# Kernel tuning notes

Hardware: AMD Instinct MI355X
Metric: run time of the kernel (lower is better)

The kernel has to match this reference:

```python
import jax, jax.numpy as jnp
import numpy as np

N_NODES = 50000
N_EDGES = 800000
NFEAT, NHID, NCLASS = 512, 128, 40


def _glorot(key, fan_in, fan_out):
    # mimics the usual GCN uniform init: U(-1/sqrt(fan_out), 1/sqrt(fan_out))
    stdv = 1.0 / np.sqrt(fan_out)
    return jax.random.uniform(key, (fan_in, fan_out), jnp.float32, -stdv, stdv)


def setup_inputs() -> dict:
    key = jax.random.key(0)
    ks = jax.random.split(key, 8)
    x = jax.random.normal(ks[0], (N_NODES, NFEAT), jnp.float32)
    edge_src = jax.random.randint(ks[1], (N_EDGES,), 0, N_NODES)
    edge_dst = jax.random.randint(ks[2], (N_EDGES,), 0, N_NODES)
    edge_weight = jax.random.uniform(ks[3], (N_EDGES,), jnp.float32)
    W1 = _glorot(ks[4], NFEAT, NHID)
    b1 = jnp.zeros((NHID,), jnp.float32)
    W2 = _glorot(ks[5], NHID, NCLASS)
    b2 = jnp.zeros((NCLASS,), jnp.float32)
    return {"x": x, "edge_src": edge_src, "edge_dst": edge_dst,
            "edge_weight": edge_weight, "W1": W1, "b1": b1, "W2": W2, "b2": b2}


def _gcn_layer(x, W, b, edge_src, edge_dst, edge_weight):
    # support = x @ W ; out = spmm(adj, support) + b
    support = x @ W                                   # [N, F_out]
    msgs = support[edge_src] * edge_weight[:, None]   # [E, F_out]
    agg = jax.ops.segment_sum(msgs, edge_dst, num_segments=N_NODES)
    return agg + b


def reference(x, edge_src, edge_dst, edge_weight, W1, b1, W2, b2):
    h = _gcn_layer(x, W1, b1, edge_src, edge_dst, edge_weight)
    h = jax.nn.relu(h)
    # F.dropout(training=False) -> identity in eval mode
    out = _gcn_layer(h, W2, b2, edge_src, edge_dst, edge_weight)
    return out
```

## Files before the change

### kernel.cpp

```cpp
#include <hip/hip_runtime.h>


#define F0 512
#define F1 128
#define F2 40
#define F2P 48

typedef short bf16x8 __attribute__((ext_vector_type(8)));
typedef float f32x4 __attribute__((ext_vector_type(4)));

static __device__ __forceinline__ unsigned short f2b(float f){
    union { float f; unsigned int u; } x; x.f = f;
    unsigned int u = x.u;
    unsigned int r = (u + 0x7fffu + ((u >> 16) & 1u)) >> 16;
    return (unsigned short)r;
}
static __device__ __forceinline__ unsigned short f2b_fast(float f){
    return (unsigned short)((__float_as_uint(f) + 0x8000u) >> 16);
}
static __device__ __forceinline__ unsigned int pack2(float a, float b){
    unsigned int ua = __float_as_uint(a) + 0x8000u;
    unsigned int ub = __float_as_uint(b) + 0x8000u;
    return __builtin_amdgcn_perm(ub, ua, 0x07060302u);
}
static __device__ __forceinline__ bf16x8 pack8(float4 v0, float4 v1){
    union { bf16x8 v; unsigned int d[4]; } r;
    r.d[0] = pack2(v0.x, v0.y);
    r.d[1] = pack2(v0.z, v0.w);
    r.d[2] = pack2(v1.x, v1.y);
    r.d[3] = pack2(v1.z, v1.w);
    return r.v;
}
static __device__ __forceinline__ float b2f(unsigned short h){
    union { unsigned int u; float f; } x; x.u = ((unsigned int)h) << 16; return x.f;
}
static __device__ __forceinline__ unsigned short f2h(float f){
    union { _Float16 h; unsigned short u; } x; x.h = (_Float16)f; return x.u;
}
static __device__ __forceinline__ float h2f(unsigned short u){
    union { unsigned short u; _Float16 h; } x; x.u = u; return (float)x.h;
}

__global__ void prep_w(const float* __restrict__ W1, const float* __restrict__ W2,
                       unsigned short* __restrict__ W1t, unsigned short* __restrict__ W2t,
                       int* __restrict__ cnt8, int n8){
    int idx = blockIdx.x*256 + threadIdx.x;
    if (idx < n8) cnt8[idx] = 0;
    if (idx < F0*F1){
        int k = idx >> 7, n = idx & 127;
        W1t[(size_t)n*F0 + k] = f2b(W1[idx]);
    } else if (idx < F0*F1 + F2P*F1){
        int j = idx - F0*F1;
        int n = j >> 7, k = j & 127;
        float v = (n < F2) ? W2[(size_t)k*F2 + n] : 0.f;
        W2t[j] = f2b(v);
    }
}

__global__ void hist_kernel(const int* __restrict__ dst, int* __restrict__ cnt8,
                            unsigned short* __restrict__ slot, int E){
    int e = blockIdx.x*256 + threadIdx.x;
    if (e < E){
        int d = dst[e];
        int s = e & 7;
        slot[e] = (unsigned short)atomicAdd(&cnt8[d*8 + s], 1);
    }
}

__global__ void scan1_kernel(const int* __restrict__ cnt8, int* __restrict__ offs,
                             unsigned short* __restrict__ lsp, int* __restrict__ bsum, int n){
    __shared__ int sd[256];
    int tid = threadIdx.x;
    int base = blockIdx.x*1024 + tid*4;
    int t[4];
    #pragma unroll
    for (int j=0;j<4;j++){
        int node = base+j;
        int tot = 0;
        if (node < n){
            int4 c0 = *(const int4*)&cnt8[(size_t)node*8];
            int4 c1 = *(const int4*)&cnt8[(size_t)node*8+4];
            unsigned short lp0=0, lp1, lp2, lp3, lp4, lp5, lp6, lp7;
            int run = c0.x; lp1=(unsigned short)run;
            run += c0.y; lp2=(unsigned short)run;
            run += c0.z; lp3=(unsigned short)run;
            run += c0.w; lp4=(unsigned short)run;
            run += c1.x; lp5=(unsigned short)run;
            run += c1.y; lp6=(unsigned short)run;
            run += c1.z; lp7=(unsigned short)run;
            run += c1.w; tot = run;
            ushort4 a, b;
            a.x=lp0; a.y=lp1; a.z=lp2; a.w=lp3;
            b.x=lp4; b.y=lp5; b.z=lp6; b.w=lp7;
            *(ushort4*)&lsp[(size_t)node*8]   = a;
            *(ushort4*)&lsp[(size_t)node*8+4] = b;
        }
        t[j] = tot;
    }
    int v1=t[0], v2=t[0]+t[1], v3=v2+t[2];
    int s = v3+t[3];
    sd[tid]=s; __syncthreads();
    for (int off=1; off<256; off<<=1){
        int tt = (tid>=off)? sd[tid-off] : 0;
        __syncthreads();
        sd[tid] += tt;
        __syncthreads();
    }
    int excl = sd[tid] - s;
    if (base+0<n) offs[base+0]=excl;
    if (base+1<n) offs[base+1]=excl+v1;
    if (base+2<n) offs[base+2]=excl+v2;
    if (base+3<n) offs[base+3]=excl+v3;
    if (tid==255) bsum[blockIdx.x]=sd[255];
}

__global__ void scan3_kernel(int* __restrict__ offs, int* __restrict__ sbase,
                             const unsigned short* __restrict__ lsp,
                             const int* __restrict__ bsum, int n, int E, int nb){
    __shared__ int sexcl;
    int tid = threadIdx.x;
    if (tid < 64){
        int v = (tid < nb) ? bsum[tid] : 0;
        int orig = v;
        #pragma unroll
        for (int off=1; off<64; off<<=1){
            int t = __shfl_up(v, off);
            if (tid >= off) v += t;
        }
        int g = blockIdx.x >> 2;
        if (tid == g) sexcl = v - orig;
    }
    __syncthreads();
    int i = blockIdx.x*256 + tid;
    if (i<n){
        int o = offs[i] + sexcl;
        offs[i] = o;
        ushort4 a = *(const ushort4*)&lsp[(size_t)i*8];
        ushort4 b = *(const ushort4*)&lsp[(size_t)i*8+4];
        int4 s0, s1;
        s0.x=o+a.x; s0.y=o+a.y; s0.z=o+a.z; s0.w=o+a.w;
        s1.x=o+b.x; s1.y=o+b.y; s1.z=o+b.z; s1.w=o+b.w;
        *(int4*)&sbase[(size_t)i*8]   = s0;
        *(int4*)&sbase[(size_t)i*8+4] = s1;
    }
    if (i==0) offs[n]=E;
}

__global__ void scatter_kernel(const int* __restrict__ src, const int* __restrict__ dst,
                               const float* __restrict__ w,
                               const int* __restrict__ sbase,
                               const unsigned short* __restrict__ slot,
                               unsigned int* __restrict__ edges, int E){
    int e = blockIdx.x*256+threadIdx.x;
    if (e<E){
        int d = dst[e];
        int pos = sbase[d*8 + (e & 7)] + (int)slot[e];
        edges[pos] = ((unsigned int)src[e] << 16) | (unsigned int)f2h(w[e]);
    }
}

__global__ __launch_bounds__(256) void gemm1_mfma(const float* __restrict__ X,
                                                  const unsigned short* __restrict__ W1t,
                                                  unsigned short* __restrict__ S1, int M){
    __shared__ unsigned short sB[128*136];
    int tid = threadIdx.x;
    int wave = tid >> 6, lane = tid & 63;
    int quad = lane >> 4, l16 = lane & 15;
    int row0 = blockIdx.x * 64;
    int myrow = row0 + wave*16 + l16;
    int arow = min(myrow, M-1);
    const float* xrow = X + (size_t)arow * F0;

    f32x4 acc[8];
    #pragma unroll
    for (int c=0;c<8;c++) acc[c] = (f32x4){0.f,0.f,0.f,0.f};

    float4 aq[4][2];
    #pragma unroll
    for (int s=0;s<4;s++){
        aq[s][0] = *(const float4*)(xrow + s*32 + quad*8);
        aq[s][1] = *(const float4*)(xrow + s*32 + quad*8 + 4);
    }

    for (int p = 0; p < 4; p++){
        __syncthreads();
        #pragma unroll
        for (int i=0;i<8;i++){
            int idx = tid + i*256;
            int nn = idx >> 4, c8 = idx & 15;
            *(float4*)&sB[nn*136 + c8*8] =
                *(const float4*)&W1t[(size_t)nn*F0 + p*128 + c8*8];
        }
        __syncthreads();
        float4 nq[4][2];
        if (p < 3){
            const float* nx = xrow + (p+1)*128;
            #pragma unroll
            for (int s=0;s<4;s++){
                nq[s][0] = *(const float4*)(nx + s*32 + quad*8);
                nq[s][1] = *(const float4*)(nx + s*32 + quad*8 + 4);
            }
        }
        #pragma unroll
        for (int s=0;s<4;s++){
            bf16x8 af = pack8(aq[s][0], aq[s][1]);
            #pragma unroll
            for (int c=0;c<8;c++){
                bf16x8 b = *(bf16x8*)&sB[(c*16 + l16)*136 + s*32 + quad*8];
                acc[c] = __builtin_amdgcn_mfma_f32_16x16x32_bf16(af, b, acc[c], 0, 0, 0);
            }
        }
        if (p < 3){
            #pragma unroll
            for (int s=0;s<4;s++){ aq[s][0]=nq[s][0]; aq[s][1]=nq[s][1]; }
        }
    }
    #pragma unroll
    for (int c=0;c<8;c++){
        #pragma unroll
        for (int r=0;r<4;r++){
            int grow = row0 + wave*16 + quad*4 + r;
            if (grow < M) S1[(size_t)grow*F1 + c*16 + l16] = f2b_fast(acc[c][r]);
        }
    }
}

__global__ void agg1_kernel(const unsigned short* __restrict__ S1, const int* __restrict__ offs,
                            const unsigned int* __restrict__ edges,
                            const float* __restrict__ b1, unsigned short* __restrict__ H, int n){
    int node = blockIdx.x*4 + (threadIdx.x >> 6);
    int lane = threadIdx.x & 63;
    if (node >= n) return;
    int half = lane >> 5, fl = lane & 31;
    int e0 = offs[node], e1 = offs[node+1];
    double a0=0.0, a1=0.0, a2=0.0, a3=0.0;
    int e = e0;
    for (; e+8 <= e1; e += 8){
        unsigned int rA = edges[e   + half];
        unsigned int rB = edges[e+2 + half];
        unsigned int rC = edges[e+4 + half];
        unsigned int rD = edges[e+6 + half];
        ushort4 vA = *(const ushort4*)&S1[((size_t)(rA>>16))*F1 + fl*4];
        ushort4 vB = *(const ushort4*)&S1[((size_t)(rB>>16))*F1 + fl*4];
        ushort4 vC = *(const ushort4*)&S1[((size_t)(rC>>16))*F1 + fl*4];
        ushort4 vD = *(const ushort4*)&S1[((size_t)(rD>>16))*F1 + fl*4];
        double wA = h2f((unsigned short)rA), wB = h2f((unsigned short)rB);
        double wC = h2f((unsigned short)rC), wD = h2f((unsigned short)rD);
        a0 += wA*b2f(vA.x) + wB*b2f(vB.x) + wC*b2f(vC.x) + wD*b2f(vD.x);
        a1 += wA*b2f(vA.y) + wB*b2f(vB.y) + wC*b2f(vC.y) + wD*b2f(vD.y);
        a2 += wA*b2f(vA.z) + wB*b2f(vB.z) + wC*b2f(vC.z) + wD*b2f(vD.z);
        a3 += wA*b2f(vA.w) + wB*b2f(vB.w) + wC*b2f(vC.w) + wD*b2f(vD.w);
    }
    for (; e < e1; e += 2){
        int ee = e + half;
        if (ee < e1){
            unsigned int r = edges[ee];
            ushort4 v = *(const ushort4*)&S1[((size_t)(r>>16))*F1 + fl*4];
            double w = h2f((unsigned short)r);
            a0 += w*b2f(v.x); a1 += w*b2f(v.y); a2 += w*b2f(v.z); a3 += w*b2f(v.w);
        }
    }
    a0 += __shfl_down(a0, 32);
    a1 += __shfl_down(a1, 32);
    a2 += __shfl_down(a2, 32);
    a3 += __shfl_down(a3, 32);
    if (lane < 32){
        float4 bb = *(const float4*)&b1[fl*4];
        float o0 = (float)(a0 + (double)bb.x);
        float o1 = (float)(a1 + (double)bb.y);
        float o2 = (float)(a2 + (double)bb.z);
        float o3 = (float)(a3 + (double)bb.w);
        o0 = o0>0.f?o0:0.f; o1 = o1>0.f?o1:0.f;
        o2 = o2>0.f?o2:0.f; o3 = o3>0.f?o3:0.f;
        union { ushort4 v; unsigned int d[2]; } o;
        o.d[0] = pack2(o0, o1);
        o.d[1] = pack2(o2, o3);
        *(ushort4*)&H[(size_t)node*F1 + fl*4] = o.v;
    }
}

__global__ __launch_bounds__(256) void gemm2_mfma(const unsigned short* __restrict__ H,
                                                  const unsigned short* __restrict__ W2t,
                                                  unsigned short* __restrict__ S2, int M){
    __shared__ unsigned short sB[48][136];
    int tid = threadIdx.x;
    int wave = tid >> 6, lane = tid & 63;
    int quad = lane >> 4, l16 = lane & 15;
    for (int i = tid; i < 48*16; i += 256){
        int nn = i >> 4, p = i & 15;
        *(float4*)&sB[nn][p*8] = *(const float4*)&W2t[(size_t)nn*F1 + p*8];
    }
    int row0 = blockIdx.x * 64;
    int myrow = row0 + wave*16 + l16;
    int arow = min(myrow, M-1);
    const unsigned short* hrow = H + (size_t)arow * F1;
    bf16x8 a[4];
    #pragma unroll
    for (int ks=0; ks<4; ks++) a[ks] = *(const bf16x8*)(hrow + ks*32 + quad*8);
    __syncthreads();
    f32x4 acc[3];
    #pragma unroll
    for (int c=0;c<3;c++) acc[c] = (f32x4){0.f,0.f,0.f,0.f};
    #pragma unroll
    for (int ks=0; ks<4; ks++){
        #pragma unroll
        for (int c=0;c<3;c++){
            bf16x8 b = *(bf16x8*)&sB[c*16 + l16][ks*32 + quad*8];
            acc[c] = __builtin_amdgcn_mfma_f32_16x16x32_bf16(a[ks], b, acc[c], 0, 0, 0);
        }
    }
    #pragma unroll
    for (int c=0;c<3;c++){
        #pragma unroll
        for (int r=0;r<4;r++){
            int grow = row0 + wave*16 + quad*4 + r;
            if (grow < M) S2[(size_t)grow*F2P + c*16 + l16] = f2b_fast(acc[c][r]);
        }
    }
}

__global__ void agg2_kernel(const unsigned short* __restrict__ S2, const int* __restrict__ offs,
                            const unsigned int* __restrict__ edges,
                            const float* __restrict__ b2, float* __restrict__ out, int n){
    int node = blockIdx.x*4 + (threadIdx.x >> 6);
    int lane = threadIdx.x & 63;
    if (node >= n) return;
    int grp = lane >> 4, gl = lane & 15;
    bool act = gl < 10;
    int e0 = offs[node], e1 = offs[node+1];
    double a0=0.0, a1=0.0, a2=0.0, a3=0.0;
    for (int e = e0; e < e1; e += 4){
        int ee = e + grp;
        if (ee < e1 && act){
            unsigned int r = edges[ee];
            ushort4 v = *(const ushort4*)&S2[((size_t)(r>>16))*F2P + gl*4];
            double w = h2f((unsigned short)r);
            a0 += w*b2f(v.x); a1 += w*b2f(v.y); a2 += w*b2f(v.z); a3 += w*b2f(v.w);
        }
    }
    a0 += __shfl_down(a0, 32); a0 += __shfl_down(a0, 16);
    a1 += __shfl_down(a1, 32); a1 += __shfl_down(a1, 16);
    a2 += __shfl_down(a2, 32); a2 += __shfl_down(a2, 16);
    a3 += __shfl_down(a3, 32); a3 += __shfl_down(a3, 16);
    if (lane < 10){
        float4 bb = *(const float4*)&b2[lane*4];
        float4 o;
        o.x = (float)(a0 + (double)bb.x);
        o.y = (float)(a1 + (double)bb.y);
        o.z = (float)(a2 + (double)bb.z);
        o.w = (float)(a3 + (double)bb.w);
        *(float4*)&out[(size_t)node*F2 + lane*4] = o;
    }
}

extern "C" void kernel_launch(void* const* d_in, const int* in_sizes, int n_in,
                              void* d_out, int out_size, void* d_ws, size_t ws_size,
                              hipStream_t stream){
    const float* x    = (const float*)d_in[0];
    const int*   esrc = (const int*)d_in[1];
    const int*   edst = (const int*)d_in[2];
    const float* ew   = (const float*)d_in[3];
    const float* W1   = (const float*)d_in[4];
    const float* b1   = (const float*)d_in[5];
    const float* W2   = (const float*)d_in[6];
    const float* b2   = (const float*)d_in[7];
    float* out = (float*)d_out;
    int N = in_sizes[0] / F0;
    int E = in_sizes[1];

    char* ws = (char*)d_ws;
    size_t off = 0;
    auto alloc = [&](size_t bytes)->void*{
        void* p = ws + off; off += (bytes + 255) & ~(size_t)255; return p;
    };
    unsigned short* S1 = (unsigned short*)alloc(sizeof(unsigned short)*(size_t)N*F1);
    unsigned short* H  = (unsigned short*)alloc(sizeof(unsigned short)*(size_t)N*F1);
    unsigned short* S2 = (unsigned short*)alloc(sizeof(unsigned short)*(size_t)N*F2P);
    unsigned short* W1t = (unsigned short*)alloc(sizeof(unsigned short)*F1*F0);
    unsigned short* W2t = (unsigned short*)alloc(sizeof(unsigned short)*F2P*F1);
    int*   offs  = (int*)alloc(sizeof(int)*(size_t)(N+1));
    int*   cnt8  = (int*)alloc(sizeof(int)*(size_t)N*8);
    int*   sbase = (int*)alloc(sizeof(int)*(size_t)N*8);
    unsigned short* lsp  = (unsigned short*)alloc(sizeof(unsigned short)*(size_t)N*8);
    unsigned short* slot = (unsigned short*)alloc(sizeof(unsigned short)*(size_t)E);
    unsigned int* edges = (unsigned int*)alloc(sizeof(unsigned int)*(size_t)E);
    int*   bsum  = (int*)alloc(sizeof(int)*64);

    int n8 = N*8;
    int prep_items = n8 > (F0*F1 + F2P*F1) ? n8 : (F0*F1 + F2P*F1);
    prep_w<<<(prep_items+255)/256,256,0,stream>>>(W1, W2, W1t, W2t, cnt8, n8);

    hist_kernel<<<(E+255)/256,256,0,stream>>>(edst, cnt8, slot, E);
    int nb = (N+1023)/1024;
    scan1_kernel<<<nb,256,0,stream>>>(cnt8, offs, lsp, bsum, N);
    scan3_kernel<<<(N+255)/256,256,0,stream>>>(offs, sbase, lsp, bsum, N, E, nb);
    scatter_kernel<<<(E+255)/256,256,0,stream>>>(esrc, edst, ew, sbase, slot, edges, E);

    gemm1_mfma<<<(N+63)/64,256,0,stream>>>(x, W1t, S1, N);
    agg1_kernel<<<(N+3)/4,256,0,stream>>>(S1, offs, edges, b1, H, N);
    gemm2_mfma<<<(N+63)/64,256,0,stream>>>(H, W2t, S2, N);
    agg2_kernel<<<(N+3)/4,256,0,stream>>>(S2, offs, edges, b2, out, N);
}
```

Measured before the change: 322.6 us.

## Fuse layer-1 aggregation with layer-2 GEMM and drop sbase array

Merges agg1 and gemm2 into one kernel. Each block aggregates 16 nodes into a shared-memory tile, then wave 0 runs the MFMA against W2t read straight from global memory, so the H intermediate never goes through global memory. It also removes the per-slot sbase array: scatter now computes positions from offs plus lsp, which cuts scan3's writes. The cost is that three of four waves sit idle during the small GEMM, and the scatter kernel does one extra indexed read.

```diff
diff --git a/kernel.cpp b/kernel.cpp
--- a/kernel.cpp
+++ b/kernel.cpp
@@ -80,7 +80,7 @@
         if (node < n){
             int4 c0 = *(const int4*)&cnt8[(size_t)node*8];
             int4 c1 = *(const int4*)&cnt8[(size_t)node*8+4];
-            unsigned short lp0=0, lp1, lp2, lp3, lp4, lp5, lp6, lp7;
+            unsigned short lp1,lp2,lp3,lp4,lp5,lp6,lp7;
             int run = c0.x; lp1=(unsigned short)run;
             run += c0.y; lp2=(unsigned short)run;
             run += c0.z; lp3=(unsigned short)run;
@@ -90,7 +90,7 @@
             run += c1.z; lp7=(unsigned short)run;
             run += c1.w; tot = run;
             ushort4 a, b;
-            a.x=lp0; a.y=lp1; a.z=lp2; a.w=lp3;
+            a.x=0;   a.y=lp1; a.z=lp2; a.w=lp3;
             b.x=lp4; b.y=lp5; b.z=lp6; b.w=lp7;
             *(ushort4*)&lsp[(size_t)node*8]   = a;
             *(ushort4*)&lsp[(size_t)node*8+4] = b;
@@ -114,9 +114,8 @@
     if (tid==255) bsum[blockIdx.x]=sd[255];
 }
 
-__global__ void scan3_kernel(int* __restrict__ offs, int* __restrict__ sbase,
-                             const unsigned short* __restrict__ lsp,
-                             const int* __restrict__ bsum, int n, int E, int nb){
+__global__ void scan3_kernel(int* __restrict__ offs, const int* __restrict__ bsum,
+                             int n, int E, int nb){
     __shared__ int sexcl;
     int tid = threadIdx.x;
     if (tid < 64){
@@ -132,29 +131,20 @@
     }
     __syncthreads();
     int i = blockIdx.x*256 + tid;
-    if (i<n){
-        int o = offs[i] + sexcl;
-        offs[i] = o;
-        ushort4 a = *(const ushort4*)&lsp[(size_t)i*8];
-        ushort4 b = *(const ushort4*)&lsp[(size_t)i*8+4];
-        int4 s0, s1;
-        s0.x=o+a.x; s0.y=o+a.y; s0.z=o+a.z; s0.w=o+a.w;
-        s1.x=o+b.x; s1.y=o+b.y; s1.z=o+b.z; s1.w=o+b.w;
-        *(int4*)&sbase[(size_t)i*8]   = s0;
-        *(int4*)&sbase[(size_t)i*8+4] = s1;
-    }
+    if (i<n) offs[i] += sexcl;
     if (i==0) offs[n]=E;
 }
 
 __global__ void scatter_kernel(const int* __restrict__ src, const int* __restrict__ dst,
                                const float* __restrict__ w,
-                               const int* __restrict__ sbase,
+                               const int* __restrict__ offs,
+                               const unsigned short* __restrict__ lsp,
                                const unsigned short* __restrict__ slot,
                                unsigned int* __restrict__ edges, int E){
     int e = blockIdx.x*256+threadIdx.x;
     if (e<E){
         int d = dst[e];
-        int pos = sbase[d*8 + (e & 7)] + (int)slot[e];
+        int pos = offs[d] + (int)lsp[d*8 + (e & 7)] + (int)slot[e];
         edges[pos] = ((unsigned int)src[e] << 16) | (unsigned int)f2h(w[e]);
     }
 }
@@ -225,96 +215,94 @@
     }
 }
 
-__global__ void agg1_kernel(const unsigned short* __restrict__ S1, const int* __restrict__ offs,
-                            const unsigned int* __restrict__ edges,
-                            const float* __restrict__ b1, unsigned short* __restrict__ H, int n){
-    int node = blockIdx.x*4 + (threadIdx.x >> 6);
-    int lane = threadIdx.x & 63;
-    if (node >= n) return;
-    int half = lane >> 5, fl = lane & 31;
-    int e0 = offs[node], e1 = offs[node+1];
-    double a0=0.0, a1=0.0, a2=0.0, a3=0.0;
-    int e = e0;
-    for (; e+8 <= e1; e += 8){
-        unsigned int rA = edges[e   + half];
-        unsigned int rB = edges[e+2 + half];
-        unsigned int rC = edges[e+4 + half];
-        unsigned int rD = edges[e+6 + half];
-        ushort4 vA = *(const ushort4*)&S1[((size_t)(rA>>16))*F1 + fl*4];
-        ushort4 vB = *(const ushort4*)&S1[((size_t)(rB>>16))*F1 + fl*4];
-        ushort4 vC = *(const ushort4*)&S1[((size_t)(rC>>16))*F1 + fl*4];
-        ushort4 vD = *(const ushort4*)&S1[((size_t)(rD>>16))*F1 + fl*4];
-        double wA = h2f((unsigned short)rA), wB = h2f((unsigned short)rB);
-        double wC = h2f((unsigned short)rC), wD = h2f((unsigned short)rD);
-        a0 += wA*b2f(vA.x) + wB*b2f(vB.x) + wC*b2f(vC.x) + wD*b2f(vD.x);
-        a1 += wA*b2f(vA.y) + wB*b2f(vB.y) + wC*b2f(vC.y) + wD*b2f(vD.y);
-        a2 += wA*b2f(vA.z) + wB*b2f(vB.z) + wC*b2f(vC.z) + wD*b2f(vD.z);
-        a3 += wA*b2f(vA.w) + wB*b2f(vB.w) + wC*b2f(vC.w) + wD*b2f(vD.w);
-    }
-    for (; e < e1; e += 2){
-        int ee = e + half;
-        if (ee < e1){
-            unsigned int r = edges[ee];
-            ushort4 v = *(const ushort4*)&S1[((size_t)(r>>16))*F1 + fl*4];
-            double w = h2f((unsigned short)r);
-            a0 += w*b2f(v.x); a1 += w*b2f(v.y); a2 += w*b2f(v.z); a3 += w*b2f(v.w);
-        }
-    }
-    a0 += __shfl_down(a0, 32);
-    a1 += __shfl_down(a1, 32);
-    a2 += __shfl_down(a2, 32);
-    a3 += __shfl_down(a3, 32);
-    if (lane < 32){
-        float4 bb = *(const float4*)&b1[fl*4];
-        float o0 = (float)(a0 + (double)bb.x);
-        float o1 = (float)(a1 + (double)bb.y);
-        float o2 = (float)(a2 + (double)bb.z);
-        float o3 = (float)(a3 + (double)bb.w);
-        o0 = o0>0.f?o0:0.f; o1 = o1>0.f?o1:0.f;
-        o2 = o2>0.f?o2:0.f; o3 = o3>0.f?o3:0.f;
-        union { ushort4 v; unsigned int d[2]; } o;
-        o.d[0] = pack2(o0, o1);
-        o.d[1] = pack2(o2, o3);
-        *(ushort4*)&H[(size_t)node*F1 + fl*4] = o.v;
-    }
-}
-
-__global__ __launch_bounds__(256) void gemm2_mfma(const unsigned short* __restrict__ H,
+__global__ __launch_bounds__(256) void agg1_gemm2(const unsigned short* __restrict__ S1,
+                                                  const int* __restrict__ offs,
+                                                  const unsigned int* __restrict__ edges,
+                                                  const float* __restrict__ b1,
                                                   const unsigned short* __restrict__ W2t,
-                                                  unsigned short* __restrict__ S2, int M){
-    __shared__ unsigned short sB[48][136];
+                                                  unsigned short* __restrict__ S2, int n){
+    __shared__ unsigned short hT[16*136];
     int tid = threadIdx.x;
     int wave = tid >> 6, lane = tid & 63;
-    int quad = lane >> 4, l16 = lane & 15;
-    for (int i = tid; i < 48*16; i += 256){
-        int nn = i >> 4, p = i & 15;
-        *(float4*)&sB[nn][p*8] = *(const float4*)&W2t[(size_t)nn*F1 + p*8];
-    }
-    int row0 = blockIdx.x * 64;
-    int myrow = row0 + wave*16 + l16;
-    int arow = min(myrow, M-1);
-    const unsigned short* hrow = H + (size_t)arow * F1;
-    bf16x8 a[4];
-    #pragma unroll
-    for (int ks=0; ks<4; ks++) a[ks] = *(const bf16x8*)(hrow + ks*32 + quad*8);
+    int half = lane >> 5, fl = lane & 31;
+    int nodeBase = blockIdx.x * 16;
+
+    float4 bb;
+    if (lane < 32) bb = *(const float4*)&b1[fl*4];
+
+    #pragma unroll
+    for (int j=0;j<4;j++){
+        int ln = wave*4 + j;
+        int node = nodeBase + ln;
+        double a0=0.0, a1=0.0, a2=0.0, a3=0.0;
+        if (node < n){
+            int e0 = offs[node], e1 = offs[node+1];
+            int e = e0;
+            for (; e+8 <= e1; e += 8){
+                unsigned int rA = edges[e   + half];
+                unsigned int rB = edges[e+2 + half];
+                unsigned int rC = edges[e+4 + half];
+                unsigned int rD = edges[e+6 + half];
+                ushort4 vA = *(const ushort4*)&S1[((size_t)(rA>>16))*F1 + fl*4];
+                ushort4 vB = *(const ushort4*)&S1[((size_t)(rB>>16))*F1 + fl*4];
+                ushort4 vC = *(const ushort4*)&S1[((size_t)(rC>>16))*F1 + fl*4];
+                ushort4 vD = *(const ushort4*)&S1[((size_t)(rD>>16))*F1 + fl*4];
+                double wA = h2f((unsigned short)rA), wB = h2f((unsigned short)rB);
+                double wC = h2f((unsigned short)rC), wD = h2f((unsigned short)rD);
+                a0 += wA*b2f(vA.x) + wB*b2f(vB.x) + wC*b2f(vC.x) + wD*b2f(vD.x);
+                a1 += wA*b2f(vA.y) + wB*b2f(vB.y) + wC*b2f(vC.y) + wD*b2f(vD.y);
+                a2 += wA*b2f(vA.z) + wB*b2f(vB.z) + wC*b2f(vC.z) + wD*b2f(vD.z);
+                a3 += wA*b2f(vA.w) + wB*b2f(vB.w) + wC*b2f(vC.w) + wD*b2f(vD.w);
+            }
+            for (; e < e1; e += 2){
+                int ee = e + half;
+                if (ee < e1){
+                    unsigned int r = edges[ee];
+                    ushort4 v = *(const ushort4*)&S1[((size_t)(r>>16))*F1 + fl*4];
+                    double w = h2f((unsigned short)r);
+                    a0 += w*b2f(v.x); a1 += w*b2f(v.y); a2 += w*b2f(v.z); a3 += w*b2f(v.w);
+                }
+            }
+        }
+        a0 += __shfl_down(a0, 32);
+        a1 += __shfl_down(a1, 32);
+        a2 += __shfl_down(a2, 32);
+        a3 += __shfl_down(a3, 32);
+        if (lane < 32){
+            float o0 = (float)(a0 + (double)bb.x);
+            float o1 = (float)(a1 + (double)bb.y);
+            float o2 = (float)(a2 + (double)bb.z);
+            float o3 = (float)(a3 + (double)bb.w);
+            o0 = o0>0.f?o0:0.f; o1 = o1>0.f?o1:0.f;
+            o2 = o2>0.f?o2:0.f; o3 = o3>0.f?o3:0.f;
+            union { ushort4 v; unsigned int d[2]; } o;
+            o.d[0] = pack2(o0, o1);
+            o.d[1] = pack2(o2, o3);
+            *(ushort4*)&hT[ln*136 + fl*4] = o.v;
+        }
+    }
     __syncthreads();
-    f32x4 acc[3];
-    #pragma unroll
-    for (int c=0;c<3;c++) acc[c] = (f32x4){0.f,0.f,0.f,0.f};
-    #pragma unroll
-    for (int ks=0; ks<4; ks++){
+    if (wave == 0){
+        int quad = lane >> 4, l16 = lane & 15;
+        f32x4 acc[3];
+        #pragma unroll
+        for (int c=0;c<3;c++) acc[c] = (f32x4){0.f,0.f,0.f,0.f};
+        #pragma unroll
+        for (int ks=0; ks<4; ks++){
+            bf16x8 a = *(const bf16x8*)&hT[l16*136 + ks*32 + quad*8];
+            #pragma unroll
+            for (int c=0;c<3;c++){
+                bf16x8 b = *(const bf16x8*)&W2t[(size_t)(c*16 + l16)*F1 + ks*32 + quad*8];
+                acc[c] = __builtin_amdgcn_mfma_f32_16x16x32_bf16(a, b, acc[c], 0, 0, 0);
+            }
+        }
         #pragma unroll
         for (int c=0;c<3;c++){
-            bf16x8 b = *(bf16x8*)&sB[c*16 + l16][ks*32 + quad*8];
-            acc[c] = __builtin_amdgcn_mfma_f32_16x16x32_bf16(a[ks], b, acc[c], 0, 0, 0);
-        }
-    }
-    #pragma unroll
-    for (int c=0;c<3;c++){
-        #pragma unroll
-        for (int r=0;r<4;r++){
-            int grow = row0 + wave*16 + quad*4 + r;
-            if (grow < M) S2[(size_t)grow*F2P + c*16 + l16] = f2b_fast(acc[c][r]);
+            #pragma unroll
+            for (int r=0;r<4;r++){
+                int grow = nodeBase + quad*4 + r;
+                if (grow < n) S2[(size_t)grow*F2P + c*16 + l16] = f2b_fast(acc[c][r]);
+            }
         }
     }
 }
@@ -374,13 +362,11 @@
         void* p = ws + off; off += (bytes + 255) & ~(size_t)255; return p;
     };
     unsigned short* S1 = (unsigned short*)alloc(sizeof(unsigned short)*(size_t)N*F1);
-    unsigned short* H  = (unsigned short*)alloc(sizeof(unsigned short)*(size_t)N*F1);
     unsigned short* S2 = (unsigned short*)alloc(sizeof(unsigned short)*(size_t)N*F2P);
     unsigned short* W1t = (unsigned short*)alloc(sizeof(unsigned short)*F1*F0);
     unsigned short* W2t = (unsigned short*)alloc(sizeof(unsigned short)*F2P*F1);
     int*   offs  = (int*)alloc(sizeof(int)*(size_t)(N+1));
     int*   cnt8  = (int*)alloc(sizeof(int)*(size_t)N*8);
-    int*   sbase = (int*)alloc(sizeof(int)*(size_t)N*8);
     unsigned short* lsp  = (unsigned short*)alloc(sizeof(unsigned short)*(size_t)N*8);
     unsigned short* slot = (unsigned short*)alloc(sizeof(unsigned short)*(size_t)E);
     unsigned int* edges = (unsigned int*)alloc(sizeof(unsigned int)*(size_t)E);
@@ -393,11 +379,10 @@
     hist_kernel<<<(E+255)/256,256,0,stream>>>(edst, cnt8, slot, E);
     int nb = (N+1023)/1024;
     scan1_kernel<<<nb,256,0,stream>>>(cnt8, offs, lsp, bsum, N);
-    scan3_kernel<<<(N+255)/256,256,0,stream>>>(offs, sbase, lsp, bsum, N, E, nb);
-    scatter_kernel<<<(E+255)/256,256,0,stream>>>(esrc, edst, ew, sbase, slot, edges, E);
+    scan3_kernel<<<(N+255)/256,256,0,stream>>>(offs, bsum, N, E, nb);
+    scatter_kernel<<<(E+255)/256,256,0,stream>>>(esrc, edst, ew, offs, lsp, slot, edges, E);
 
     gemm1_mfma<<<(N+63)/64,256,0,stream>>>(x, W1t, S1, N);
-    agg1_kernel<<<(N+3)/4,256,0,stream>>>(S1, offs, edges, b1, H, N);
-    gemm2_mfma<<<(N+63)/64,256,0,stream>>>(H, W2t, S2, N);
+    agg1_gemm2<<<(N+15)/16,256,0,stream>>>(S1, offs, edges, b1, W2t, S2, N);
     agg2_kernel<<<(N+3)/4,256,0,stream>>>(S2, offs, edges, b2, out, N);
 }
```

Result: slower. 335.8 us (+4.1%).
